# Optimization experiments

Measured on AMD Instinct MI355X. Metric: run time of the kernel, lower is better.

The kernel has to match this reference:

```python
import jax, jax.numpy as jnp
import numpy as np

ATTR_LEN = [2, 4, 4, 8]  # sums to 18 = MLP output dim; prod = 256 cases
USER_EMB_DIM = 256
B = 8192


def build_cases(attr_len):
    # Cartesian product of per-attribute one-hots -> [prod(attr_len), sum(attr_len)]
    out = np.eye(attr_len[0], dtype=np.float32)
    for n in attr_len[1:]:
        m = np.eye(n, dtype=np.float32)
        out = np.concatenate(
            [np.repeat(out, n, axis=0), np.tile(m, (out.shape[0], 1))], axis=1)
    return out


def setup_inputs() -> dict:
    key = jax.random.key(0)
    ks = jax.random.split(key, 8)
    d = USER_EMB_DIM
    x = jax.random.normal(ks[0], (B, d), dtype=jnp.float32)
    y = jax.random.uniform(ks[1], (B, 18), dtype=jnp.float32)
    # nn.Linear-style params (scaled normals)
    W1 = jax.random.normal(ks[2], (d, 50), dtype=jnp.float32) / np.sqrt(d)
    b1 = jnp.zeros((50,), dtype=jnp.float32)
    W2 = jax.random.normal(ks[3], (50, 32), dtype=jnp.float32) / np.sqrt(50.0)
    b2 = jnp.zeros((32,), dtype=jnp.float32)
    W3 = jax.random.normal(ks[4], (32, 18), dtype=jnp.float32) / np.sqrt(32.0)
    b3 = jnp.zeros((18,), dtype=jnp.float32)
    cases = jnp.asarray(build_cases(ATTR_LEN))  # [256, 18]
    return {"x": x, "y": y, "W1": W1, "b1": b1, "W2": W2, "b2": b2,
            "W3": W3, "b3": b3, "cases": cases}


def reference(x, y, W1, b1, W2, b2, W3, b3, cases):
    # MLP: user_emb_dim -> 50 -> 32 -> 18, sigmoid activations on hidden layers
    h = jax.nn.sigmoid(x @ W1 + b1)
    h = jax.nn.sigmoid(h @ W2 + b2)
    W_user = h @ W3 + b3                                  # [B, 18]
    # Partition function over all combinatorial label cases, fused into one
    # GEMM + logsumexp (original loops over cases with exp+accumulate).
    log_denom = jax.nn.logsumexp(W_user @ cases.T, axis=1)  # [B]
    # obj_i = exp(sum_j W_user[i].y[j]) / denom_i ; loss = -sum log obj
    S = jnp.sum(W_user @ y.T, axis=1)                     # [B] (via [B,B] mm, as original)
    loss = -jnp.sum(S - log_denom)
    # 'logit' in the original is W_user detached to numpy; return the array.
    return W_user, loss
```

## Files before the change

kernel.cpp:

```cpp
#include <hip/hip_runtime.h>

#define NB   8192
#define ND   256
#define NH1  50
#define NH2  32
#define NH3  18
#define RPB  16
#define NBLK (NB / RPB)
#define W1TS 260
#define WSS  40


__device__ __forceinline__ float sigmoidf_fast(float v) {
    return 1.0f / (1.0f + __expf(-v));
}

__global__ __launch_bounds__(256) void fused_main(
    const float* __restrict__ x, const float* __restrict__ y,
    const float* __restrict__ W1, const float* __restrict__ b1,
    const float* __restrict__ W2, const float* __restrict__ b2,
    const float* __restrict__ W3, const float* __restrict__ b3,
    float* __restrict__ out, float* __restrict__ ws)
{
    __shared__ float w1t[NH1 * W1TS];
    __shared__ float w2l[NH1 * NH2];
    __shared__ float w3l[NH2 * NH3];
    __shared__ float h2l[RPB][NH2 + 2];
    __shared__ float wul[RPB][NH3 + 1];

    const int t    = threadIdx.x;
    const int row  = t >> 4;
    const int ksl  = t & 15;
    const int grow = blockIdx.x * RPB + row;

    const float* xrow = x + (size_t)grow * ND + ksl * 4;
    const float4 xv0 = *reinterpret_cast<const float4*>(xrow + 0);
    const float4 xv1 = *reinterpret_cast<const float4*>(xrow + 64);
    const float4 xv2 = *reinterpret_cast<const float4*>(xrow + 128);
    const float4 xv3 = *reinterpret_cast<const float4*>(xrow + 192);

    for (int e = t; e < ND * NH1; e += 256) {
        int k = e / NH1;
        int j = e - k * NH1;
        w1t[j * W1TS + k] = W1[e];
    }
    for (int e = t; e < NH1 * NH2; e += 256) w2l[e] = W2[e];
    for (int e = t; e < NH2 * NH3; e += 256) w3l[e] = W3[e];
    __syncthreads();

    float h1[NH1];
#pragma unroll
    for (int j = 0; j < NH1; ++j) {
        const float* wj = &w1t[j * W1TS + ksl * 4];
        const float4 w0 = *reinterpret_cast<const float4*>(wj + 0);
        const float4 w1v = *reinterpret_cast<const float4*>(wj + 64);
        const float4 w2v = *reinterpret_cast<const float4*>(wj + 128);
        const float4 w3v = *reinterpret_cast<const float4*>(wj + 192);
        float a;
        a = xv0.x * w0.x;
        a = fmaf(xv0.y, w0.y, a);
        a = fmaf(xv0.z, w0.z, a);
        a = fmaf(xv0.w, w0.w, a);
        a = fmaf(xv1.x, w1v.x, a);
        a = fmaf(xv1.y, w1v.y, a);
        a = fmaf(xv1.z, w1v.z, a);
        a = fmaf(xv1.w, w1v.w, a);
        a = fmaf(xv2.x, w2v.x, a);
        a = fmaf(xv2.y, w2v.y, a);
        a = fmaf(xv2.z, w2v.z, a);
        a = fmaf(xv2.w, w2v.w, a);
        a = fmaf(xv3.x, w3v.x, a);
        a = fmaf(xv3.y, w3v.y, a);
        a = fmaf(xv3.z, w3v.z, a);
        a = fmaf(xv3.w, w3v.w, a);
        h1[j] = a;
    }
#pragma unroll
    for (int j = 0; j < NH1; ++j) {
        float v = h1[j];
        v += __shfl_xor(v, 1, 64);
        v += __shfl_xor(v, 2, 64);
        v += __shfl_xor(v, 4, 64);
        v += __shfl_xor(v, 8, 64);
        h1[j] = sigmoidf_fast(v + b1[j]);
    }

    {
        const float2 bb = *reinterpret_cast<const float2*>(b2 + 2 * ksl);
        float h2a = bb.x, h2b = bb.y;
#pragma unroll
        for (int j = 0; j < NH1; ++j) {
            const float2 w = *reinterpret_cast<const float2*>(&w2l[j * NH2 + 2 * ksl]);
            h2a = fmaf(h1[j], w.x, h2a);
            h2b = fmaf(h1[j], w.y, h2b);
        }
        h2a = sigmoidf_fast(h2a);
        h2b = sigmoidf_fast(h2b);
        *reinterpret_cast<float2*>(&h2l[row][2 * ksl]) = make_float2(h2a, h2b);
    }
    __syncthreads();

    {
        float a0 = b3[ksl];
        float a1 = (ksl < 2) ? b3[16 + ksl] : 0.0f;
#pragma unroll
        for (int j = 0; j < NH2; ++j) {
            const float h = h2l[row][j];
            a0 = fmaf(h, w3l[j * NH3 + ksl], a0);
            if (ksl < 2) a1 = fmaf(h, w3l[j * NH3 + 16 + ksl], a1);
        }
        wul[row][ksl] = a0;
        out[(size_t)grow * NH3 + ksl] = a0;
        if (ksl < 2) {
            wul[row][16 + ksl] = a1;
            out[(size_t)grow * NH3 + 16 + ksl] = a1;
        }
    }
    __syncthreads();

    if (t < 64) {
        const bool act = t < RPB;
        float wv[NH3], yv[NH3];
        float ld = 0.0f;
        if (act) {
            const float* yrow = y + (size_t)(blockIdx.x * RPB + t) * NH3;
#pragma unroll
            for (int c = 0; c < NH3; ++c) {
                wv[c] = wul[t][c];
                yv[c] = yrow[c];
            }
            float m = fmaxf(wv[0], wv[1]);
            ld += m + __logf(__expf(wv[0] - m) + __expf(wv[1] - m));
            m = fmaxf(fmaxf(wv[2], wv[3]), fmaxf(wv[4], wv[5]));
            ld += m + __logf(__expf(wv[2] - m) + __expf(wv[3] - m) +
                             __expf(wv[4] - m) + __expf(wv[5] - m));
            m = fmaxf(fmaxf(wv[6], wv[7]), fmaxf(wv[8], wv[9]));
            ld += m + __logf(__expf(wv[6] - m) + __expf(wv[7] - m) +
                             __expf(wv[8] - m) + __expf(wv[9] - m));
            m = wv[10];
#pragma unroll
            for (int i = 11; i < NH3; ++i) m = fmaxf(m, wv[i]);
            float s = 0.0f;
#pragma unroll
            for (int i = 10; i < NH3; ++i) s += __expf(wv[i] - m);
            ld += m + __logf(s);
        } else {
#pragma unroll
            for (int c = 0; c < NH3; ++c) { wv[c] = 0.0f; yv[c] = 0.0f; }
        }

        ld += __shfl_xor(ld, 1, 64);
        ld += __shfl_xor(ld, 2, 64);
        ld += __shfl_xor(ld, 4, 64);
        ld += __shfl_xor(ld, 8, 64);
#pragma unroll
        for (int c = 0; c < NH3; ++c) {
            float v = wv[c];
            v += __shfl_xor(v, 1, 64);
            v += __shfl_xor(v, 2, 64);
            v += __shfl_xor(v, 4, 64);
            v += __shfl_xor(v, 8, 64);
            wv[c] = v;
            float u = yv[c];
            u += __shfl_xor(u, 1, 64);
            u += __shfl_xor(u, 2, 64);
            u += __shfl_xor(u, 4, 64);
            u += __shfl_xor(u, 8, 64);
            yv[c] = u;
        }
        if (t == 0) {
            float* slot = ws + (size_t)blockIdx.x * WSS;
#pragma unroll
            for (int c = 0; c < NH3; ++c) {
                slot[c]       = yv[c];
                slot[NH3 + c] = wv[c];
            }
            slot[36] = ld;
        }
    }
}

__global__ __launch_bounds__(256) void finalize_loss(
    const float* __restrict__ ws, float* __restrict__ out)
{
    __shared__ double part[4][37];
    const int t = threadIdx.x;
    const int w = t >> 6, l = t & 63;
    if (l < 37) {
        double a = 0.0;
        for (int b = w * (NBLK / 4); b < (w + 1) * (NBLK / 4); ++b)
            a += (double)ws[(size_t)b * WSS + l];
        part[w][l] = a;
    }
    __syncthreads();
    if (t == 0) {
        double tot[37];
#pragma unroll
        for (int c = 0; c < 37; ++c)
            tot[c] = part[0][c] + part[1][c] + part[2][c] + part[3][c];
        double s = 0.0;
#pragma unroll
        for (int c = 0; c < NH3; ++c)
            s += tot[NH3 + c] * tot[c];
        out[(size_t)NB * NH3] = (float)(-(s - tot[36]));
    }
}

extern "C" void kernel_launch(void* const* d_in, const int* in_sizes, int n_in,
                              void* d_out, int out_size, void* d_ws, size_t ws_size,
                              hipStream_t stream) {
    const float* x  = (const float*)d_in[0];
    const float* y  = (const float*)d_in[1];
    const float* W1 = (const float*)d_in[2];
    const float* b1 = (const float*)d_in[3];
    const float* W2 = (const float*)d_in[4];
    const float* b2 = (const float*)d_in[5];
    const float* W3 = (const float*)d_in[6];
    const float* b3 = (const float*)d_in[7];
    float* out = (float*)d_out;
    float* ws  = (float*)d_ws;

    fused_main<<<dim3(NBLK), dim3(256), 0, stream>>>(x, y, W1, b1, W2, b2, W3, b3, out, ws);
    finalize_loss<<<dim3(1), dim3(256), 0, stream>>>(ws, out);
}
```

Before: 103.3 us.

## Restructure layer-1 GEMV to two rows per thread with DPP reductions

Layer 1 is remapped so each 32-lane group handles two rows with 8 k-values per lane, and each W1 LDS load is reused for both rows. The 16-lane shuffle reductions become DPP row-reductions, and the sigmoid outputs go to a shared h1 buffer instead of staying in 50 per-thread registers. h2 and W_user staging now alias the W1 shared tile, which shrinks LDS to raise occupancy. The cost is an extra barrier and a single writer lane per pair, and the DPP control masks must reduce correctly across the 32-lane group.

```diff
diff --git a/kernel.cpp b/kernel.cpp
--- a/kernel.cpp
+++ b/kernel.cpp
@@ -13,6 +13,12 @@
 
 __device__ __forceinline__ float sigmoidf_fast(float v) {
     return 1.0f / (1.0f + __expf(-v));
+}
+
+template <int CTRL, int RMASK>
+__device__ __forceinline__ float dpp_add(float v) {
+    int d = __builtin_amdgcn_update_dpp(0, __float_as_int(v), CTRL, RMASK, 0xF, true);
+    return v + __int_as_float(d);
 }
 
 __global__ __launch_bounds__(256) void fused_main(
@@ -25,19 +31,22 @@
     __shared__ float w1t[NH1 * W1TS];
     __shared__ float w2l[NH1 * NH2];
     __shared__ float w3l[NH2 * NH3];
-    __shared__ float h2l[RPB][NH2 + 2];
-    __shared__ float wul[RPB][NH3 + 1];
-
-    const int t    = threadIdx.x;
-    const int row  = t >> 4;
-    const int ksl  = t & 15;
-    const int grow = blockIdx.x * RPB + row;
-
-    const float* xrow = x + (size_t)grow * ND + ksl * 4;
-    const float4 xv0 = *reinterpret_cast<const float4*>(xrow + 0);
-    const float4 xv1 = *reinterpret_cast<const float4*>(xrow + 64);
-    const float4 xv2 = *reinterpret_cast<const float4*>(xrow + 128);
-    const float4 xv3 = *reinterpret_cast<const float4*>(xrow + 192);
+    __shared__ float h1l[NH1][RPB];
+    float (*h2l)[NH2 + 2] = (float (*)[NH2 + 2])(w1t);
+    float (*wul)[NH3 + 1] = (float (*)[NH3 + 1])(w1t + 600);
+
+    const int t   = threadIdx.x;
+    const int ksl = t & 31;
+    const int rp  = t >> 5;
+    const int c16 = t & 15;
+    const int row = t >> 4;
+    const int rbase = blockIdx.x * RPB;
+
+    const float* xr = x + (size_t)(rbase + rp * 2) * ND + ksl * 8;
+    const float4 xa0 = *reinterpret_cast<const float4*>(xr);
+    const float4 xa1 = *reinterpret_cast<const float4*>(xr + 4);
+    const float4 xb0 = *reinterpret_cast<const float4*>(xr + ND);
+    const float4 xb1 = *reinterpret_cast<const float4*>(xr + ND + 4);
 
     for (int e = t; e < ND * NH1; e += 256) {
         int k = e / NH1;
@@ -48,72 +57,72 @@
     for (int e = t; e < NH2 * NH3; e += 256) w3l[e] = W3[e];
     __syncthreads();
 
-    float h1[NH1];
-#pragma unroll
-    for (int j = 0; j < NH1; ++j) {
-        const float* wj = &w1t[j * W1TS + ksl * 4];
-        const float4 w0 = *reinterpret_cast<const float4*>(wj + 0);
-        const float4 w1v = *reinterpret_cast<const float4*>(wj + 64);
-        const float4 w2v = *reinterpret_cast<const float4*>(wj + 128);
-        const float4 w3v = *reinterpret_cast<const float4*>(wj + 192);
-        float a;
-        a = xv0.x * w0.x;
-        a = fmaf(xv0.y, w0.y, a);
-        a = fmaf(xv0.z, w0.z, a);
-        a = fmaf(xv0.w, w0.w, a);
-        a = fmaf(xv1.x, w1v.x, a);
-        a = fmaf(xv1.y, w1v.y, a);
-        a = fmaf(xv1.z, w1v.z, a);
-        a = fmaf(xv1.w, w1v.w, a);
-        a = fmaf(xv2.x, w2v.x, a);
-        a = fmaf(xv2.y, w2v.y, a);
-        a = fmaf(xv2.z, w2v.z, a);
-        a = fmaf(xv2.w, w2v.w, a);
-        a = fmaf(xv3.x, w3v.x, a);
-        a = fmaf(xv3.y, w3v.y, a);
-        a = fmaf(xv3.z, w3v.z, a);
-        a = fmaf(xv3.w, w3v.w, a);
-        h1[j] = a;
-    }
-#pragma unroll
-    for (int j = 0; j < NH1; ++j) {
-        float v = h1[j];
-        v += __shfl_xor(v, 1, 64);
-        v += __shfl_xor(v, 2, 64);
-        v += __shfl_xor(v, 4, 64);
-        v += __shfl_xor(v, 8, 64);
-        h1[j] = sigmoidf_fast(v + b1[j]);
-    }
-
     {
-        const float2 bb = *reinterpret_cast<const float2*>(b2 + 2 * ksl);
+        const float* wb = &w1t[ksl * 8];
+#pragma unroll 2
+        for (int j = 0; j < NH1; ++j) {
+            const float4 w0 = *reinterpret_cast<const float4*>(wb + j * W1TS);
+            const float4 w1v = *reinterpret_cast<const float4*>(wb + j * W1TS + 4);
+            float s0 = xa0.x * w0.x;
+            s0 = fmaf(xa0.y, w0.y, s0);
+            s0 = fmaf(xa0.z, w0.z, s0);
+            s0 = fmaf(xa0.w, w0.w, s0);
+            s0 = fmaf(xa1.x, w1v.x, s0);
+            s0 = fmaf(xa1.y, w1v.y, s0);
+            s0 = fmaf(xa1.z, w1v.z, s0);
+            s0 = fmaf(xa1.w, w1v.w, s0);
+            float s1 = xb0.x * w0.x;
+            s1 = fmaf(xb0.y, w0.y, s1);
+            s1 = fmaf(xb0.z, w0.z, s1);
+            s1 = fmaf(xb0.w, w0.w, s1);
+            s1 = fmaf(xb1.x, w1v.x, s1);
+            s1 = fmaf(xb1.y, w1v.y, s1);
+            s1 = fmaf(xb1.z, w1v.z, s1);
+            s1 = fmaf(xb1.w, w1v.w, s1);
+            s0 = dpp_add<0xB1, 0xF>(s0);  s1 = dpp_add<0xB1, 0xF>(s1);
+            s0 = dpp_add<0x4E, 0xF>(s0);  s1 = dpp_add<0x4E, 0xF>(s1);
+            s0 = dpp_add<0x141, 0xF>(s0); s1 = dpp_add<0x141, 0xF>(s1);
+            s0 = dpp_add<0x140, 0xF>(s0); s1 = dpp_add<0x140, 0xF>(s1);
+            s0 = dpp_add<0x142, 0xA>(s0); s1 = dpp_add<0x142, 0xA>(s1);
+            if ((t & 31) == 16) {
+                const float bj = b1[j];
+                *reinterpret_cast<float2*>(&h1l[j][rp * 2]) =
+                    make_float2(sigmoidf_fast(s0 + bj), sigmoidf_fast(s1 + bj));
+            }
+        }
+    }
+    __syncthreads();
+
+    {
+        const float2 bb = *reinterpret_cast<const float2*>(b2 + 2 * c16);
         float h2a = bb.x, h2b = bb.y;
 #pragma unroll
         for (int j = 0; j < NH1; ++j) {
-            const float2 w = *reinterpret_cast<const float2*>(&w2l[j * NH2 + 2 * ksl]);
-            h2a = fmaf(h1[j], w.x, h2a);
-            h2b = fmaf(h1[j], w.y, h2b);
-        }
-        h2a = sigmoidf_fast(h2a);
-        h2b = sigmoidf_fast(h2b);
-        *reinterpret_cast<float2*>(&h2l[row][2 * ksl]) = make_float2(h2a, h2b);
+            const float h = h1l[j][row];
+            const float2 w = *reinterpret_cast<const float2*>(&w2l[j * NH2 + 2 * c16]);
+            h2a = fmaf(h, w.x, h2a);
+            h2b = fmaf(h, w.y, h2b);
+        }
+        *reinterpret_cast<float2*>(&h2l[row][2 * c16]) =
+            make_float2(sigmoidf_fast(h2a), sigmoidf_fast(h2b));
     }
     __syncthreads();
 
     {
-        float a0 = b3[ksl];
-        float a1 = (ksl < 2) ? b3[16 + ksl] : 0.0f;
+        float a0 = b3[c16];
+        float a1 = (c16 < 2) ? b3[16 + c16] : 0.0f;
 #pragma unroll
         for (int j = 0; j < NH2; ++j) {
             const float h = h2l[row][j];
-            a0 = fmaf(h, w3l[j * NH3 + ksl], a0);
-            if (ksl < 2) a1 = fmaf(h, w3l[j * NH3 + 16 + ksl], a1);
-        }
-        wul[row][ksl] = a0;
-        out[(size_t)grow * NH3 + ksl] = a0;
-        if (ksl < 2) {
-            wul[row][16 + ksl] = a1;
-            out[(size_t)grow * NH3 + 16 + ksl] = a1;
+            a0 = fmaf(h, w3l[j * NH3 + c16], a0);
+            if (c16 < 2) a1 = fmaf(h, w3l[j * NH3 + 16 + c16], a1);
+        }
+        const int grow = rbase + row;
+        wul[row][c16] = a0;
+        out[(size_t)grow * NH3 + c16] = a0;
+        if (c16 < 2) {
+            wul[row][16 + c16] = a1;
+            out[(size_t)grow * NH3 + 16 + c16] = a1;
         }
     }
     __syncthreads();
@@ -123,7 +132,7 @@
         float wv[NH3], yv[NH3];
         float ld = 0.0f;
         if (act) {
-            const float* yrow = y + (size_t)(blockIdx.x * RPB + t) * NH3;
+            const float* yrow = y + (size_t)(rbase + t) * NH3;
 #pragma unroll
             for (int c = 0; c < NH3; ++c) {
                 wv[c] = wul[t][c];
```

After: 104.3 us. About the same (+1.0%).
